# Optimization experiments

Hardware: AMD Instinct MI355X
Metric: run time of the kernel (lower is better)

Reference implementation:

```python
import jax, jax.numpy as jnp
import numpy as np

NUM_HEADS = 16
D_MODEL = 1024
D_K = 64
D_V = 64
NEG_INF = -1e9


def setup_inputs() -> dict:
    key = jax.random.key(0)
    ks = jax.random.split(key, 7)
    B, S = 2, 2048
    Q = jax.random.normal(ks[0], (B, S, D_MODEL), dtype=jnp.float32)
    K = jax.random.normal(ks[1], (B, S, D_MODEL), dtype=jnp.float32)
    V = jax.random.normal(ks[2], (B, S, D_MODEL), dtype=jnp.float32)
    s = 1.0 / np.sqrt(D_MODEL)
    W_q = jax.random.normal(ks[3], (D_MODEL, D_K * NUM_HEADS), dtype=jnp.float32) * s
    W_k = jax.random.normal(ks[4], (D_MODEL, D_K), dtype=jnp.float32) * s
    W_v = jax.random.normal(ks[5], (D_MODEL, D_V), dtype=jnp.float32) * s
    W_o = jax.random.normal(ks[6], (D_V * NUM_HEADS, D_MODEL), dtype=jnp.float32) * (1.0 / np.sqrt(D_V * NUM_HEADS))
    return {"Q": Q, "K": K, "V": V, "W_q": W_q, "W_k": W_k, "W_v": W_v, "W_o": W_o}


def reference(Q, K, V, W_q, W_k, W_v, W_o):
    B, Sq, _ = Q.shape
    Sk = K.shape[1]
    # projections: Q -> per-head, K/V -> single shared head (MQA)
    q = (Q @ W_q).reshape(B, Sq, NUM_HEADS, D_K).transpose(0, 2, 1, 3)  # [B,H,Sq,Dk]
    k = K @ W_k  # [B,Sk,Dk]
    v = V @ W_v  # [B,Sk,Dv]
    scores = jnp.einsum('bhqd,bkd->bhqk', q, k) / jnp.sqrt(jnp.float32(D_K))
    causal = jnp.tril(jnp.ones((Sq, Sk), dtype=bool))  # [Sq,Sk]
    scores = jnp.where(causal[None, None], scores, NEG_INF)
    attn = jax.nn.softmax(scores, axis=-1)  # [B,H,Sq,Sk]
    out = jnp.einsum('bhqk,bkd->bhqd', attn, v)  # [B,H,Sq,Dv]
    out = out.transpose(0, 2, 1, 3).reshape(B, Sq, NUM_HEADS * D_V)
    return out @ W_o
```

## Files before the change

### kernel.cpp

```cpp
#include <hip/hip_runtime.h>
#include <hip/hip_bf16.h>
#include <cstdint>

typedef __bf16 bf16_t;
typedef __bf16 bf16x8 __attribute__((ext_vector_type(8)));
typedef __bf16 bf16x4 __attribute__((ext_vector_type(4)));
typedef float  floatx4 __attribute__((ext_vector_type(4)));

__device__ __forceinline__ bf16_t f2bf(float x) { return (bf16_t)x; }

__device__ __forceinline__ void gll16(const void* g, void* l) {
  __builtin_amdgcn_global_load_lds((const __attribute__((address_space(1))) void*)g,
                                   (__attribute__((address_space(3))) void*)l, 16, 0, 0);
}

#define S_LEN 2048
#define NHEAD 16

__global__ __launch_bounds__(256) void transpose_all(const float* __restrict__ Wq,
                                                     const float* __restrict__ Wo,
                                                     const float* __restrict__ Wk,
                                                     const float* __restrict__ Wv,
                                                     bf16_t* __restrict__ Wqt,
                                                     bf16_t* __restrict__ Wot,
                                                     bf16_t* __restrict__ Wkt,
                                                     bf16_t* __restrict__ Wvt) {
  const int bid = blockIdx.x;
  const float* W; bf16_t* Wt; int n0, k0, N;
  if (bid < 2048) {
    int z = bid >> 10, rem = bid & 1023;
    W = z ? Wo : Wq; Wt = z ? Wot : Wqt;
    n0 = (rem & 31) * 32; k0 = (rem >> 5) * 32; N = 1024;
  } else {
    int b2 = bid - 2048, z = b2 >> 6, rem = b2 & 63;
    W = z ? Wv : Wk; Wt = z ? Wvt : Wkt;
    n0 = (rem & 1) * 32; k0 = (rem >> 1) * 32; N = 64;
  }
  const int K = 1024;
  __shared__ float tile[32][33];
  int tx = threadIdx.x & 31, ty = threadIdx.x >> 5;
#pragma unroll
  for (int r = 0; r < 4; ++r)
    tile[ty + 8 * r][tx] = W[(size_t)(k0 + ty + 8 * r) * N + n0 + tx];
  __syncthreads();
#pragma unroll
  for (int r = 0; r < 4; ++r)
    Wt[(size_t)(n0 + ty + 8 * r) * K + k0 + tx] = f2bf(tile[tx][ty + 8 * r]);
}

template <int OUTMODE, bool A_FP32>
__device__ __forceinline__ void gemm_body(const void* __restrict__ Ain,
                                          const bf16_t* __restrict__ Bt,
                                          void* __restrict__ Cout,
                                          int M, int N, int K,
                                          int m0, int n0,
                                          bf16_t* As, bf16_t* Bs) {
  constexpr int BK = 64;
  const int tid = threadIdx.x;
  const int wave = tid >> 6, lane = tid & 63;
  const int quad = lane >> 4, lm = lane & 15;
  const int wr = wave >> 1, wc = wave & 1;

  floatx4 acc[2][4];
#pragma unroll
  for (int i = 0; i < 2; ++i)
#pragma unroll
    for (int j = 0; j < 4; ++j) acc[i][j] = (floatx4){0.f, 0.f, 0.f, 0.f};

  for (int k0 = 0; k0 < K; k0 += BK) {
    if constexpr (A_FP32) {
#pragma unroll
      for (int rd = 0; rd < 2; ++rd) {
        int idx = rd * 256 + tid, row = idx >> 3, ch = (idx & 7) ^ (row & 7);
        const float* src = (const float*)Ain + (size_t)(m0 + row) * K + k0 + ch * 8;
        float4 f0 = *(const float4*)src;
        float4 f1 = *(const float4*)(src + 4);
        bf16x8 o;
        o[0] = f2bf(f0.x); o[1] = f2bf(f0.y); o[2] = f2bf(f0.z); o[3] = f2bf(f0.w);
        o[4] = f2bf(f1.x); o[5] = f2bf(f1.y); o[6] = f2bf(f1.z); o[7] = f2bf(f1.w);
        *(bf16x8*)&As[idx * 8] = o;
      }
    } else {
#pragma unroll
      for (int rd = 0; rd < 2; ++rd) {
        int idx = rd * 256 + tid, row = idx >> 3, ch = (idx & 7) ^ (row & 7);
        gll16((const bf16_t*)Ain + (size_t)(m0 + row) * K + k0 + ch * 8,
              As + (rd * 256 + wave * 64) * 8);
      }
    }
#pragma unroll
    for (int rd = 0; rd < 4; ++rd) {
      int idx = rd * 256 + tid, row = idx >> 3, ch = (idx & 7) ^ (row & 7);
      gll16(Bt + (size_t)(n0 + row) * K + k0 + ch * 8,
            Bs + (rd * 256 + wave * 64) * 8);
    }
    __syncthreads();
    const int sw = lm & 7;
    bf16x8 af[2][2], bfr[4][2];
#pragma unroll
    for (int i = 0; i < 2; ++i) {
      const bf16_t* base = &As[(wr * 32 + i * 16 + lm) * BK];
      af[i][0] = *(const bf16x8*)(base + ((quad ^ sw) * 8));
      af[i][1] = *(const bf16x8*)(base + (((4 + quad) ^ sw) * 8));
    }
#pragma unroll
    for (int j = 0; j < 4; ++j) {
      const bf16_t* base = &Bs[(wc * 64 + j * 16 + lm) * BK];
      bfr[j][0] = *(const bf16x8*)(base + ((quad ^ sw) * 8));
      bfr[j][1] = *(const bf16x8*)(base + (((4 + quad) ^ sw) * 8));
    }
#pragma unroll
    for (int ks = 0; ks < 2; ++ks)
#pragma unroll
      for (int i = 0; i < 2; ++i)
#pragma unroll
        for (int j = 0; j < 4; ++j)
          acc[i][j] = __builtin_amdgcn_mfma_f32_16x16x32_bf16(af[i][ks], bfr[j][ks],
                                                              acc[i][j], 0, 0, 0);
    __syncthreads();
  }
#pragma unroll
  for (int i = 0; i < 2; ++i) {
#pragma unroll
    for (int j = 0; j < 4; ++j) {
      int row0 = m0 + wr * 32 + i * 16 + quad * 4;
      int col = n0 + wc * 64 + j * 16 + lm;
#pragma unroll
      for (int r = 0; r < 4; ++r) {
        if constexpr (OUTMODE == 3)
          ((bf16_t*)Cout)[(size_t)(row0 + r) * N + col] = f2bf(acc[i][j][r] * 0.125f);
        else
          ((float*)Cout)[(size_t)(row0 + r) * N + col] = acc[i][j][r];
      }
    }
  }
}

__device__ __forceinline__ void kv_body(const float* __restrict__ A32,
                                        const bf16_t* __restrict__ Bt,
                                        bf16_t* __restrict__ kp,
                                        bf16_t* __restrict__ vpt,
                                        int M, int K, int m0, int isV,
                                        bf16_t* As, bf16_t* Bs) {
  constexpr int BK = 32, LDK = 40, N = 64;
  const int tid = threadIdx.x;
  const int wave = tid >> 6, lane = tid & 63;
  const int quad = lane >> 4, lm = lane & 15;
  const int wr = wave >> 1, wc = wave & 1;

  floatx4 acc[2][2];
#pragma unroll
  for (int i = 0; i < 2; ++i)
#pragma unroll
    for (int j = 0; j < 2; ++j) acc[i][j] = (floatx4){0.f, 0.f, 0.f, 0.f};

  for (int k0 = 0; k0 < K; k0 += BK) {
    {
      int row = tid >> 2, c8 = tid & 3;
      const float* src = A32 + (size_t)(m0 + row) * K + k0 + c8 * 8;
      float4 f0 = *(const float4*)src;
      float4 f1 = *(const float4*)(src + 4);
      bf16x8 o;
      o[0] = f2bf(f0.x); o[1] = f2bf(f0.y); o[2] = f2bf(f0.z); o[3] = f2bf(f0.w);
      o[4] = f2bf(f1.x); o[5] = f2bf(f1.y); o[6] = f2bf(f1.z); o[7] = f2bf(f1.w);
      *(bf16x8*)&As[row * LDK + c8 * 8] = o;
    }
    {
      int row = tid >> 2, c8 = tid & 3;
      *(bf16x8*)&Bs[row * LDK + c8 * 8] =
          *(const bf16x8*)(Bt + (size_t)row * K + k0 + c8 * 8);
    }
    __syncthreads();
    bf16x8 af[2], bfr[2];
#pragma unroll
    for (int i = 0; i < 2; ++i)
      af[i] = *(const bf16x8*)&As[(wr * 32 + i * 16 + lm) * LDK + quad * 8];
#pragma unroll
    for (int j = 0; j < 2; ++j)
      bfr[j] = *(const bf16x8*)&Bs[(wc * 32 + j * 16 + lm) * LDK + quad * 8];
#pragma unroll
    for (int i = 0; i < 2; ++i)
#pragma unroll
      for (int j = 0; j < 2; ++j)
        acc[i][j] = __builtin_amdgcn_mfma_f32_16x16x32_bf16(af[i], bfr[j],
                                                            acc[i][j], 0, 0, 0);
    __syncthreads();
  }
#pragma unroll
  for (int i = 0; i < 2; ++i) {
#pragma unroll
    for (int j = 0; j < 2; ++j) {
      int row0 = m0 + wr * 32 + i * 16 + quad * 4;
      int col = wc * 32 + j * 16 + lm;
      if (isV) {
        bf16x4 o;
#pragma unroll
        for (int r = 0; r < 4; ++r) o[r] = f2bf(acc[i][j][r]);
        *(bf16x4*)&vpt[(size_t)col * M + row0] = o;
      } else {
#pragma unroll
        for (int r = 0; r < 4; ++r)
          kp[(size_t)(row0 + r) * N + col] = f2bf(acc[i][j][r]);
      }
    }
  }
}

__global__ __launch_bounds__(256, 2) void proj_all(const float* __restrict__ Q,
                                                   const float* __restrict__ K,
                                                   const float* __restrict__ V,
                                                   const bf16_t* __restrict__ Wqt,
                                                   const bf16_t* __restrict__ Wkt,
                                                   const bf16_t* __restrict__ Wvt,
                                                   bf16_t* __restrict__ qp,
                                                   bf16_t* __restrict__ kp,
                                                   bf16_t* __restrict__ vpt,
                                                   int BS) {
  __shared__ __align__(16) bf16_t As[64 * 64];
  __shared__ __align__(16) bf16_t Bs[128 * 64];
  const int bid = blockIdx.x;
  const int nQ = (BS / 64) * 8;
  if (bid < nQ) {
    int m0 = (bid & (BS / 64 - 1)) * 64, n0 = (bid / (BS / 64)) * 128;
    gemm_body<3, true>(Q, Wqt, qp, BS, 1024, 1024, m0, n0, As, Bs);
  } else {
    int b2 = bid - nQ;
    int isV = (b2 >= BS / 64);
    int m0 = (b2 & (BS / 64 - 1)) * 64;
    kv_body(isV ? V : K, isV ? Wvt : Wkt, kp, vpt, BS, 1024, m0, isV, As, Bs);
  }
}

__global__ __launch_bounds__(256, 2) void gemm_oproj(const bf16_t* __restrict__ A,
                                                     const bf16_t* __restrict__ Bt,
                                                     float* __restrict__ Cout,
                                                     int M, int N, int K) {
  __shared__ __align__(16) bf16_t As[64 * 64];
  __shared__ __align__(16) bf16_t Bs[128 * 64];
  gemm_body<0, false>(A, Bt, Cout, M, N, K,
                      blockIdx.x * 64, blockIdx.y * 128, As, Bs);
}

__global__ __launch_bounds__(256, 2) void flash_mqa(const bf16_t* __restrict__ q,
                                                    const bf16_t* __restrict__ kk,
                                                    const bf16_t* __restrict__ vt,
                                                    bf16_t* __restrict__ Opart,
                                                    float* __restrict__ lpart,
                                                    int BStot) {
  const int c = blockIdx.x;
  int qt, s;
  if (c < 16)      { qt = c; s = 0; }
  else if (c < 48) { qt = 16 + ((c - 16) >> 1); s = (c - 16) & 1; }
  else if (c < 96) { int d = c - 48; int q3 = d / 3; qt = 32 + q3; s = d - q3 * 3; }
  else             { qt = 48 + ((c - 96) >> 2); s = (c - 96) & 3; }
  const int n = (qt >> 1) + 1;
  const int nchunks = (n + 7) >> 3;
  const int kt0 = s * 8;
  const int kt1 = (kt0 + 8 < n) ? kt0 + 8 : n;
  const int ktmax = n - 1;

  const int hg = blockIdx.y, b = blockIdx.z;
  const int tid = threadIdx.x;
  const int wave = tid >> 6, lane = tid & 63;
  const int quad = lane >> 4, lm = lane & 15;
  const int h = hg * 4 + wave;

  __shared__ __align__(16) bf16_t k_lds[2][64 * 64];
  __shared__ __align__(16) bf16_t v_lds[2][64 * 64];
  __shared__ __align__(16) bf16_t p_lds[4][32 * 64];

  const size_t bS = (size_t)b * S_LEN;
  const int qb = qt * 32;
  const int qoff = qb - ktmax * 64;
  const int sw = lm & 7;

  bf16x8 qf[2][2];
#pragma unroll
  for (int m = 0; m < 2; ++m) {
    const bf16_t* qp = q + (bS + qb + m * 16 + lm) * 1024 + h * 64;
    qf[m][0] = *(const bf16x8*)(qp + quad * 8);
    qf[m][1] = *(const bf16x8*)(qp + 32 + quad * 8);
  }
  bf16x8 onesf;
#pragma unroll
  for (int j = 0; j < 8; ++j) onesf[j] = f2bf(1.0f);

  floatx4 acc[2][4];
  floatx4 ps[2];
#pragma unroll
  for (int m = 0; m < 2; ++m) {
    ps[m] = (floatx4){0.f, 0.f, 0.f, 0.f};
#pragma unroll
    for (int t = 0; t < 4; ++t) acc[m][t] = (floatx4){0.f, 0.f, 0.f, 0.f};
  }

  bf16x8 kst[2], vst[2];
  auto load_kv = [&](int kt) {
    const int k0 = kt * 64;
#pragma unroll
    for (int it = 0; it < 2; ++it) {
      int idx = it * 256 + tid, r = idx >> 3, c8 = idx & 7;
      kst[it] = *(const bf16x8*)(kk + (bS + k0 + r) * 64 + c8 * 8);
      vst[it] = *(const bf16x8*)(vt + (size_t)r * BStot + bS + k0 + c8 * 8);
    }
  };
  auto write_kv = [&](int buf) {
#pragma unroll
    for (int it = 0; it < 2; ++it) {
      int idx = it * 256 + tid, r = idx >> 3, c8 = idx & 7;
      int addr = r * 64 + ((c8 ^ (r & 7)) * 8);
      *(bf16x8*)&k_lds[buf][addr] = kst[it];
      *(bf16x8*)&v_lds[buf][addr] = vst[it];
    }
  };

  load_kv(kt0);
  write_kv(kt0 & 1);
  __syncthreads();

  for (int kt = kt0; kt < kt1; ++kt) {
    const int cur = kt & 1;
    if (kt + 1 < kt1) load_kv(kt + 1);
    const bool diag = (kt == ktmax);

#pragma unroll
    for (int t = 0; t < 4; ++t) {
      const bf16_t* kb = &k_lds[cur][(t * 16 + lm) * 64];
      bf16x8 a0 = *(const bf16x8*)(kb + ((quad ^ sw) * 8));
      bf16x8 a1 = *(const bf16x8*)(kb + (((4 + quad) ^ sw) * 8));
      floatx4 sv[2];
#pragma unroll
      for (int m = 0; m < 2; ++m) {
        floatx4 cc = (floatx4){0.f, 0.f, 0.f, 0.f};
        cc = __builtin_amdgcn_mfma_f32_16x16x32_bf16(a0, qf[m][0], cc, 0, 0, 0);
        cc = __builtin_amdgcn_mfma_f32_16x16x32_bf16(a1, qf[m][1], cc, 0, 0, 0);
        sv[m] = cc;
      }
      if (diag) {
#pragma unroll
        for (int m = 0; m < 2; ++m) {
          int qq = qoff + m * 16 + lm;
#pragma unroll
          for (int r = 0; r < 4; ++r) {
            int kj = t * 16 + quad * 4 + r;
            sv[m][r] = (kj <= qq) ? __expf(sv[m][r]) : 0.f;
          }
        }
      } else {
#pragma unroll
        for (int m = 0; m < 2; ++m)
#pragma unroll
          for (int r = 0; r < 4; ++r) sv[m][r] = __expf(sv[m][r]);
      }
#pragma unroll
      for (int m = 0; m < 2; ++m) {
        bf16x4 pk;
#pragma unroll
        for (int r = 0; r < 4; ++r) pk[r] = f2bf(sv[m][r]);
        *(bf16x4*)&p_lds[wave][(m * 16 + lm) * 64 +
                               (((2 * t + (quad >> 1)) ^ sw) * 8) + (quad & 1) * 4] = pk;
      }
    }
    bf16x8 p0[2], p1[2];
#pragma unroll
    for (int m = 0; m < 2; ++m) {
      const bf16_t* pb = &p_lds[wave][(m * 16 + lm) * 64];
      p0[m] = *(const bf16x8*)(pb + ((quad ^ sw) * 8));
      p1[m] = *(const bf16x8*)(pb + (((4 + quad) ^ sw) * 8));
      ps[m] = __builtin_amdgcn_mfma_f32_16x16x32_bf16(p0[m], onesf, ps[m], 0, 0, 0);
      ps[m] = __builtin_amdgcn_mfma_f32_16x16x32_bf16(p1[m], onesf, ps[m], 0, 0, 0);
    }
#pragma unroll
    for (int t = 0; t < 4; ++t) {
      const bf16_t* vb = &v_lds[cur][(t * 16 + lm) * 64];
      bf16x8 v0 = *(const bf16x8*)(vb + ((quad ^ sw) * 8));
      bf16x8 v1 = *(const bf16x8*)(vb + (((4 + quad) ^ sw) * 8));
#pragma unroll
      for (int m = 0; m < 2; ++m) {
        acc[m][t] = __builtin_amdgcn_mfma_f32_16x16x32_bf16(p0[m], v0, acc[m][t], 0, 0, 0);
        acc[m][t] = __builtin_amdgcn_mfma_f32_16x16x32_bf16(p1[m], v1, acc[m][t], 0, 0, 0);
      }
    }
    if (kt + 1 < kt1) write_kv(1 - cur);
    __syncthreads();
  }

  const size_t slotO = (size_t)BStot * 1024;
  const size_t slotL = (size_t)BStot * 16;
#pragma unroll
  for (int m = 0; m < 2; ++m) {
    const int q0 = qb + m * 16 + quad * 4;
#pragma unroll
    for (int t = 0; t < 4; ++t)
#pragma unroll
      for (int r = 0; r < 4; ++r)
        Opart[s * slotO + (bS + q0 + r) * 1024 + h * 64 + t * 16 + lm] =
            f2bf(acc[m][t][r]);
    if (lm == 0)
#pragma unroll
      for (int r = 0; r < 4; ++r)
        lpart[s * slotL + (bS + q0 + r) * 16 + h] = ps[m][r];
  }
  if (s == 0) {
    for (int ss = nchunks; ss < 4; ++ss) {
#pragma unroll
      for (int m = 0; m < 2; ++m) {
        const int q0 = qb + m * 16 + quad * 4;
#pragma unroll
        for (int t = 0; t < 4; ++t)
#pragma unroll
          for (int r = 0; r < 4; ++r)
            Opart[ss * slotO + (bS + q0 + r) * 1024 + h * 64 + t * 16 + lm] = f2bf(0.f);
        if (lm == 0)
#pragma unroll
          for (int r = 0; r < 4; ++r)
            lpart[ss * slotL + (bS + q0 + r) * 16 + h] = 0.f;
      }
    }
  }
}

__global__ __launch_bounds__(256) void combine_o(const bf16_t* __restrict__ Opart,
                                                 const float* __restrict__ lpart,
                                                 bf16_t* __restrict__ Ob, int BS) {
  const int idx = (blockIdx.x * 256 + threadIdx.x) * 8;
  const int row = idx >> 10, col = idx & 1023, h = col >> 6;
  const size_t slotO = (size_t)BS * 1024;
  const size_t slotL = (size_t)BS * 16;
  float l = 0.f;
#pragma unroll
  for (int s = 0; s < 4; ++s) l += lpart[s * slotL + row * 16 + h];
  float o[8];
#pragma unroll
  for (int j = 0; j < 8; ++j) o[j] = 0.f;
#pragma unroll
  for (int s = 0; s < 4; ++s) {
    bf16x8 v = *(const bf16x8*)(Opart + s * slotO + idx);
#pragma unroll
    for (int j = 0; j < 8; ++j) o[j] += (float)v[j];
  }
  const float rl = 1.0f / l;
  bf16x8 out;
#pragma unroll
  for (int j = 0; j < 8; ++j) out[j] = f2bf(o[j] * rl);
  *(bf16x8*)(Ob + idx) = out;
}

extern "C" void kernel_launch(void* const* d_in, const int* in_sizes, int n_in,
                              void* d_out, int out_size, void* d_ws, size_t ws_size,
                              hipStream_t stream) {
  const float* Q  = (const float*)d_in[0];
  const float* K  = (const float*)d_in[1];
  const float* V  = (const float*)d_in[2];
  const float* Wq = (const float*)d_in[3];
  const float* Wk = (const float*)d_in[4];
  const float* Wv = (const float*)d_in[5];
  const float* Wo = (const float*)d_in[6];

  const int BS = in_sizes[0] / 1024;
  const int B  = BS / S_LEN;

  bf16_t* ws  = (bf16_t*)d_ws;
  bf16_t* qp  = ws;
  bf16_t* Ob  = qp  + (size_t)BS * 1024;
  bf16_t* Wqt = Ob  + (size_t)BS * 1024;
  bf16_t* Wot = Wqt + (size_t)1024 * 1024;
  bf16_t* Wkt = Wot + (size_t)1024 * 1024;
  bf16_t* Wvt = Wkt + (size_t)64 * 1024;
  bf16_t* kp  = Wvt + (size_t)64 * 1024;
  bf16_t* vpt = kp  + (size_t)BS * 64;
  bf16_t* Opart = vpt + (size_t)BS * 64;
  float*  lpart = (float*)(Opart + (size_t)4 * BS * 1024);

  transpose_all<<<2176, 256, 0, stream>>>(Wq, Wo, Wk, Wv, Wqt, Wot, Wkt, Wvt);

  proj_all<<<(BS / 64) * 8 + (BS / 64) * 2, 256, 0, stream>>>(
      Q, K, V, Wqt, Wkt, Wvt, qp, kp, vpt, BS);

  flash_mqa<<<dim3(160, NHEAD / 4, B), 256, 0, stream>>>(qp, kp, vpt, Opart, lpart, BS);

  combine_o<<<(BS * 1024) / (256 * 8), 256, 0, stream>>>(Opart, lpart, Ob, BS);

  gemm_oproj<<<dim3(BS / 64, 8), 256, 0, stream>>>(Ob, Wot, (float*)d_out, BS, 1024, 1024);
}
```

Measured before the change: 192.8 us.

## Pre-convert Q to bf16 and shrink projection GEMM tiles to 64x64

Moves the fp32-to-bf16 conversion of the Q input out of the projection GEMM into the weight-prep kernel, writing a bf16 copy to workspace so the Q projection can use async global-to-LDS loads. Both the Q projection and output projection GEMMs drop from 64x128 to 64x64 tiles, doubling the block count and raising launch bounds to 4 blocks per CU for better occupancy on 4096x1024 problems. The cost is an extra bf16 round trip of Q through memory and lower per-block data reuse from smaller tiles.

```diff
diff --git a/kernel.cpp b/kernel.cpp
--- a/kernel.cpp
+++ b/kernel.cpp
@@ -17,15 +17,29 @@
 #define S_LEN 2048
 #define NHEAD 16
 
-__global__ __launch_bounds__(256) void transpose_all(const float* __restrict__ Wq,
-                                                     const float* __restrict__ Wo,
-                                                     const float* __restrict__ Wk,
-                                                     const float* __restrict__ Wv,
-                                                     bf16_t* __restrict__ Wqt,
-                                                     bf16_t* __restrict__ Wot,
-                                                     bf16_t* __restrict__ Wkt,
-                                                     bf16_t* __restrict__ Wvt) {
+__global__ __launch_bounds__(256) void prep_all(const float* __restrict__ Wq,
+                                                const float* __restrict__ Wo,
+                                                const float* __restrict__ Wk,
+                                                const float* __restrict__ Wv,
+                                                const float* __restrict__ Q,
+                                                bf16_t* __restrict__ Wqt,
+                                                bf16_t* __restrict__ Wot,
+                                                bf16_t* __restrict__ Wkt,
+                                                bf16_t* __restrict__ Wvt,
+                                                bf16_t* __restrict__ Qb) {
   const int bid = blockIdx.x;
+  if (bid >= 2176) {
+    const int base = (bid - 2176) * 8192;
+#pragma unroll
+    for (int j = 0; j < 8; ++j) {
+      int idx = base + j * 1024 + threadIdx.x * 4;
+      float4 v = *(const float4*)(Q + idx);
+      bf16x4 o;
+      o[0] = f2bf(v.x); o[1] = f2bf(v.y); o[2] = f2bf(v.z); o[3] = f2bf(v.w);
+      *(bf16x4*)(Qb + idx) = o;
+    }
+    return;
+  }
   const float* W; bf16_t* Wt; int n0, k0, N;
   if (bid < 2048) {
     int z = bid >> 10, rem = bid & 1023;
@@ -48,64 +62,49 @@
     Wt[(size_t)(n0 + ty + 8 * r) * K + k0 + tx] = f2bf(tile[tx][ty + 8 * r]);
 }
 
-template <int OUTMODE, bool A_FP32>
-__device__ __forceinline__ void gemm_body(const void* __restrict__ Ain,
-                                          const bf16_t* __restrict__ Bt,
-                                          void* __restrict__ Cout,
-                                          int M, int N, int K,
-                                          int m0, int n0,
-                                          bf16_t* As, bf16_t* Bs) {
-  constexpr int BK = 64;
+template <int OUTMODE>
+__device__ __forceinline__ void gemm64_body(const bf16_t* __restrict__ A,
+                                            const bf16_t* __restrict__ Bt,
+                                            void* __restrict__ Cout,
+                                            int M, int N, int K,
+                                            int m0, int n0,
+                                            bf16_t* As, bf16_t* Bs) {
   const int tid = threadIdx.x;
   const int wave = tid >> 6, lane = tid & 63;
   const int quad = lane >> 4, lm = lane & 15;
   const int wr = wave >> 1, wc = wave & 1;
 
-  floatx4 acc[2][4];
+  floatx4 acc[2][2];
 #pragma unroll
   for (int i = 0; i < 2; ++i)
 #pragma unroll
-    for (int j = 0; j < 4; ++j) acc[i][j] = (floatx4){0.f, 0.f, 0.f, 0.f};
-
-  for (int k0 = 0; k0 < K; k0 += BK) {
-    if constexpr (A_FP32) {
-#pragma unroll
-      for (int rd = 0; rd < 2; ++rd) {
-        int idx = rd * 256 + tid, row = idx >> 3, ch = (idx & 7) ^ (row & 7);
-        const float* src = (const float*)Ain + (size_t)(m0 + row) * K + k0 + ch * 8;
-        float4 f0 = *(const float4*)src;
-        float4 f1 = *(const float4*)(src + 4);
-        bf16x8 o;
-        o[0] = f2bf(f0.x); o[1] = f2bf(f0.y); o[2] = f2bf(f0.z); o[3] = f2bf(f0.w);
-        o[4] = f2bf(f1.x); o[5] = f2bf(f1.y); o[6] = f2bf(f1.z); o[7] = f2bf(f1.w);
-        *(bf16x8*)&As[idx * 8] = o;
-      }
-    } else {
-#pragma unroll
-      for (int rd = 0; rd < 2; ++rd) {
-        int idx = rd * 256 + tid, row = idx >> 3, ch = (idx & 7) ^ (row & 7);
-        gll16((const bf16_t*)Ain + (size_t)(m0 + row) * K + k0 + ch * 8,
-              As + (rd * 256 + wave * 64) * 8);
-      }
-    }
-#pragma unroll
-    for (int rd = 0; rd < 4; ++rd) {
+    for (int j = 0; j < 2; ++j) acc[i][j] = (floatx4){0.f, 0.f, 0.f, 0.f};
+
+  for (int k0 = 0; k0 < K; k0 += 64) {
+#pragma unroll
+    for (int rd = 0; rd < 2; ++rd) {
+      int idx = rd * 256 + tid, row = idx >> 3, ch = (idx & 7) ^ (row & 7);
+      gll16(A + (size_t)(m0 + row) * K + k0 + ch * 8,
+            As + (rd * 256 + wave * 64) * 8);
+    }
+#pragma unroll
+    for (int rd = 0; rd < 2; ++rd) {
       int idx = rd * 256 + tid, row = idx >> 3, ch = (idx & 7) ^ (row & 7);
       gll16(Bt + (size_t)(n0 + row) * K + k0 + ch * 8,
             Bs + (rd * 256 + wave * 64) * 8);
     }
     __syncthreads();
     const int sw = lm & 7;
-    bf16x8 af[2][2], bfr[4][2];
+    bf16x8 af[2][2], bfr[2][2];
 #pragma unroll
     for (int i = 0; i < 2; ++i) {
-      const bf16_t* base = &As[(wr * 32 + i * 16 + lm) * BK];
+      const bf16_t* base = &As[(wr * 32 + i * 16 + lm) * 64];
       af[i][0] = *(const bf16x8*)(base + ((quad ^ sw) * 8));
       af[i][1] = *(const bf16x8*)(base + (((4 + quad) ^ sw) * 8));
     }
 #pragma unroll
-    for (int j = 0; j < 4; ++j) {
-      const bf16_t* base = &Bs[(wc * 64 + j * 16 + lm) * BK];
+    for (int j = 0; j < 2; ++j) {
+      const bf16_t* base = &Bs[(wc * 32 + j * 16 + lm) * 64];
       bfr[j][0] = *(const bf16x8*)(base + ((quad ^ sw) * 8));
       bfr[j][1] = *(const bf16x8*)(base + (((4 + quad) ^ sw) * 8));
     }
@@ -114,7 +113,7 @@
 #pragma unroll
       for (int i = 0; i < 2; ++i)
 #pragma unroll
-        for (int j = 0; j < 4; ++j)
+        for (int j = 0; j < 2; ++j)
           acc[i][j] = __builtin_amdgcn_mfma_f32_16x16x32_bf16(af[i][ks], bfr[j][ks],
                                                               acc[i][j], 0, 0, 0);
     __syncthreads();
@@ -122,9 +121,9 @@
 #pragma unroll
   for (int i = 0; i < 2; ++i) {
 #pragma unroll
-    for (int j = 0; j < 4; ++j) {
+    for (int j = 0; j < 2; ++j) {
       int row0 = m0 + wr * 32 + i * 16 + quad * 4;
-      int col = n0 + wc * 64 + j * 16 + lm;
+      int col = n0 + wc * 32 + j * 16 + lm;
 #pragma unroll
       for (int r = 0; r < 4; ++r) {
         if constexpr (OUTMODE == 3)
@@ -206,7 +205,7 @@
   }
 }
 
-__global__ __launch_bounds__(256, 2) void proj_all(const float* __restrict__ Q,
+__global__ __launch_bounds__(256, 4) void proj_all(const bf16_t* __restrict__ Qb,
                                                    const float* __restrict__ K,
                                                    const float* __restrict__ V,
                                                    const bf16_t* __restrict__ Wqt,
@@ -217,28 +216,28 @@
                                                    bf16_t* __restrict__ vpt,
                                                    int BS) {
   __shared__ __align__(16) bf16_t As[64 * 64];
-  __shared__ __align__(16) bf16_t Bs[128 * 64];
+  __shared__ __align__(16) bf16_t Bs[64 * 64];
   const int bid = blockIdx.x;
-  const int nQ = (BS / 64) * 8;
+  const int mB = BS / 64;
+  const int nQ = mB * 16;
   if (bid < nQ) {
-    int m0 = (bid & (BS / 64 - 1)) * 64, n0 = (bid / (BS / 64)) * 128;
-    gemm_body<3, true>(Q, Wqt, qp, BS, 1024, 1024, m0, n0, As, Bs);
+    int m0 = (bid % mB) * 64, n0 = (bid / mB) * 64;
+    gemm64_body<3>(Qb, Wqt, qp, BS, 1024, 1024, m0, n0, As, Bs);
   } else {
     int b2 = bid - nQ;
-    int isV = (b2 >= BS / 64);
-    int m0 = (b2 & (BS / 64 - 1)) * 64;
+    int isV = (b2 >= mB);
+    int m0 = (b2 % mB) * 64;
     kv_body(isV ? V : K, isV ? Wvt : Wkt, kp, vpt, BS, 1024, m0, isV, As, Bs);
   }
 }
 
-__global__ __launch_bounds__(256, 2) void gemm_oproj(const bf16_t* __restrict__ A,
+__global__ __launch_bounds__(256, 4) void gemm_oproj(const bf16_t* __restrict__ A,
                                                      const bf16_t* __restrict__ Bt,
                                                      float* __restrict__ Cout,
                                                      int M, int N, int K) {
   __shared__ __align__(16) bf16_t As[64 * 64];
-  __shared__ __align__(16) bf16_t Bs[128 * 64];
-  gemm_body<0, false>(A, Bt, Cout, M, N, K,
-                      blockIdx.x * 64, blockIdx.y * 128, As, Bs);
+  __shared__ __align__(16) bf16_t Bs[64 * 64];
+  gemm64_body<0>(A, Bt, Cout, M, N, K, blockIdx.x * 64, blockIdx.y * 64, As, Bs);
 }
 
 __global__ __launch_bounds__(256, 2) void flash_mqa(const bf16_t* __restrict__ q,
@@ -471,15 +470,17 @@
   bf16_t* vpt = kp  + (size_t)BS * 64;
   bf16_t* Opart = vpt + (size_t)BS * 64;
   float*  lpart = (float*)(Opart + (size_t)4 * BS * 1024);
-
-  transpose_all<<<2176, 256, 0, stream>>>(Wq, Wo, Wk, Wv, Wqt, Wot, Wkt, Wvt);
-
-  proj_all<<<(BS / 64) * 8 + (BS / 64) * 2, 256, 0, stream>>>(
-      Q, K, V, Wqt, Wkt, Wvt, qp, kp, vpt, BS);
+  bf16_t* Qb  = (bf16_t*)(lpart + (size_t)4 * BS * 16);
+
+  prep_all<<<2176 + BS / 8, 256, 0, stream>>>(Wq, Wo, Wk, Wv, Q,
+                                              Wqt, Wot, Wkt, Wvt, Qb);
+
+  proj_all<<<(BS / 64) * 16 + (BS / 64) * 2, 256, 0, stream>>>(
+      Qb, K, V, Wqt, Wkt, Wvt, qp, kp, vpt, BS);
 
   flash_mqa<<<dim3(160, NHEAD / 4, B), 256, 0, stream>>>(qp, kp, vpt, Opart, lpart, BS);
 
   combine_o<<<(BS * 1024) / (256 * 8), 256, 0, stream>>>(Opart, lpart, Ob, BS);
 
-  gemm_oproj<<<dim3(BS / 64, 8), 256, 0, stream>>>(Ob, Wot, (float*)d_out, BS, 1024, 1024);
-}
+  gemm_oproj<<<dim3(BS / 64, 16), 256, 0, stream>>>(Ob, Wot, (float*)d_out, BS, 1024, 1024);
+}
```

Result: no change. 194.0 us (+0.6%).
